# Kernel tuning notes

Hardware: AMD Instinct MI355X
Metric: run time of the kernel (lower is better)

## Reference

```python
import jax, jax.numpy as jnp
import numpy as np

B, S, D, H = 2, 2048, 1024, 16
DK = D // H

def setup_inputs() -> dict:
    key = jax.random.key(0)
    ks = jax.random.split(key, 8)
    scale = 1.0 / np.sqrt(D)
    return {
        "q": jax.random.normal(ks[0], (B, S, D), jnp.float32),
        "k": jax.random.normal(ks[1], (B, S, D), jnp.float32),
        "v": jax.random.normal(ks[2], (B, S, D), jnp.float32),
        "reaches": jax.random.uniform(ks[3], (B, S), jnp.float32),
        "Wq": jax.random.normal(ks[4], (D, D), jnp.float32) * scale,
        "Wk": jax.random.normal(ks[5], (D, D), jnp.float32) * scale,
        "Wv": jax.random.normal(ks[6], (D, D), jnp.float32) * scale,
        "Wo": jax.random.normal(ks[7], (D, D), jnp.float32) * scale,
    }

def _split_heads(x):
    # [B,S,D] -> [B,H,S,DK]
    return x.reshape(B, S, H, DK).transpose(0, 2, 1, 3)

def reference(q, k, v, reaches, Wq, Wk, Wv, Wo):
    # torch Linear: y = x @ W.T
    qh = _split_heads(q @ Wq.T)
    kh = _split_heads(k @ Wk.T)
    vh = _split_heads(v @ Wv.T)
    scores = jnp.einsum("bhqd,bhkd->bhqk", qh, kh) / jnp.sqrt(jnp.float32(DK))
    scores = jax.nn.softmax(scores, axis=-1)
    # post-softmax reach weighting along key axis
    scores = scores * reaches[:, None, None, :]
    # diagonal suppression: scores - scores*0.999999*eye
    scores = scores * (1.0 - 0.999999 * jnp.eye(S, dtype=scores.dtype))
    # inverted combine
    out = vh - jnp.einsum("bhqk,bhkd->bhqd", scores, vh)
    # per-position contribution rescale
    rs = reaches.sum(axis=-1, keepdims=True)
    contrib = (rs - reaches) / (rs + 1e-9) * (1.0 - reaches) * 100.0  # [B,S]
    out = out * contrib[:, None, :, None]
    concat = out.transpose(0, 2, 1, 3).reshape(B, S, D)
    return concat @ Wo.T
```

## Files before the change

### kernel.cpp

```cpp
#include <hip/hip_runtime.h>
#include <hip/hip_bf16.h>

typedef __attribute__((ext_vector_type(8))) short short8;
typedef __attribute__((ext_vector_type(4))) float f32x4;
typedef __attribute__((ext_vector_type(16))) float f32x16;
typedef unsigned short us;

#define B_ 2
#define S_ 2048
#define D_ 1024
#define H_ 16
#define DK_ 64
#define QSCALE 0.1803368867f

__device__ __forceinline__ us f2bf(float f) {
  union { float f; unsigned u; } x; x.f = f;
  unsigned r = x.u + 0x7FFFu + ((x.u >> 16) & 1u);
  return (us)(r >> 16);
}
__device__ __forceinline__ float bf2f(us h) {
  union { unsigned u; float f; } x; x.u = ((unsigned)h) << 16;
  return x.f;
}
__device__ __forceinline__ us f2bf_hw(float f) {
  __hip_bfloat16 h = __float2bfloat16(f);
  return *reinterpret_cast<us*>(&h);
}
__device__ __forceinline__ unsigned cvtpk(float lo, float hi) {
  unsigned r;
  asm("v_cvt_pk_bf16_f32 %0, %1, %2" : "=v"(r) : "v"(lo), "v"(hi));
  return r;
}

__device__ __forceinline__ void gload16(const void* g, void* l) {
  __builtin_amdgcn_global_load_lds((const __attribute__((address_space(1))) void*)g,
                                   (__attribute__((address_space(3))) void*)l, 16, 0, 0);
}

__global__ __launch_bounds__(256) void cvt_all(const float* __restrict__ q,
                                               const float* __restrict__ k,
                                               const float* __restrict__ v,
                                               const float* __restrict__ Wq,
                                               const float* __restrict__ Wk,
                                               const float* __restrict__ Wv,
                                               const float* __restrict__ Wo,
                                               us* __restrict__ oq, us* __restrict__ ok,
                                               us* __restrict__ ov, us* __restrict__ oWq,
                                               us* __restrict__ oWk, us* __restrict__ oWv,
                                               us* __restrict__ oWo) {
  int bid = blockIdx.x;
  const float* in; us* out; int off;
  if (bid < 12288) {
    int t = bid >> 12;
    in = (t == 0) ? q : (t == 1) ? k : v;
    out = (t == 0) ? oq : (t == 1) ? ok : ov;
    off = (bid & 4095) * 1024;
  } else {
    int t = (bid - 12288) >> 10;
    in = (t == 0) ? Wq : (t == 1) ? Wk : (t == 2) ? Wv : Wo;
    out = (t == 0) ? oWq : (t == 1) ? oWk : (t == 2) ? oWv : oWo;
    off = ((bid - 12288) & 1023) * 1024;
  }
  int i = off + threadIdx.x * 4;
  float4 val = *reinterpret_cast<const float4*>(in + i);
  ushort4 o;
  o.x = f2bf(val.x); o.y = f2bf(val.y); o.z = f2bf(val.z); o.w = f2bf(val.w);
  *reinterpret_cast<ushort4*>(out + i) = o;
}

__global__ __launch_bounds__(256) void rs_kernel(const float* __restrict__ reaches,
                                                 float* __restrict__ rs) {
  int b = blockIdx.x, t = threadIdx.x;
  float s = 0.f;
  for (int i = t; i < S_; i += 256) s += reaches[b * S_ + i];
  for (int o = 32; o > 0; o >>= 1) s += __shfl_down(s, o, 64);
  __shared__ float tmp[4];
  if ((t & 63) == 0) tmp[t >> 6] = s;
  __syncthreads();
  if (t == 0) rs[b] = tmp[0] + tmp[1] + tmp[2] + tmp[3];
}

__device__ __forceinline__ void gemm_core_hs(const us* __restrict__ A, const us* __restrict__ Bt,
                                             us* __restrict__ outH, float oscale) {
  __shared__ __align__(16) us lA[128 * 32];
  __shared__ __align__(16) us lB[128 * 32];
  const int tid = threadIdx.x;
  const int bm = blockIdx.x >> 3, bn = blockIdx.x & 7;
  const int w = tid >> 6, lane = tid & 63;
  const int wr = (w >> 1) * 64, wc = (w & 1) * 64;
  const int lr = lane & 15, lg = lane >> 4;

  f32x4 acc[4][4];
#pragma unroll
  for (int i = 0; i < 4; ++i)
#pragma unroll
    for (int j = 0; j < 4; ++j) acc[i][j] = (f32x4){0.f, 0.f, 0.f, 0.f};

  const int crow = lane >> 2, ce8 = (lane & 3) * 8;
  const us* A0 = A + (size_t)(bm * 128 + w * 32 + crow) * 1024 + ce8;
  const us* A1 = A0 + (size_t)16 * 1024;
  const us* B0 = Bt + (size_t)(bn * 128 + w * 32 + crow) * 1024 + ce8;
  const us* B1 = B0 + (size_t)16 * 1024;
  us* lA0 = &lA[(w * 2) * 512]; us* lA1 = lA0 + 512;
  us* lB0 = &lB[(w * 2) * 512]; us* lB1 = lB0 + 512;

  for (int kt = 0; kt < 1024; kt += 32) {
    gload16(A0 + kt, lA0);
    gload16(A1 + kt, lA1);
    gload16(B0 + kt, lB0);
    gload16(B1 + kt, lB1);
    __syncthreads();
    short8 af[4], bfr[4];
#pragma unroll
    for (int i = 0; i < 4; ++i)
      af[i] = *reinterpret_cast<const short8*>(&lA[(wr + i * 16 + lr) * 32 + lg * 8]);
#pragma unroll
    for (int j = 0; j < 4; ++j)
      bfr[j] = *reinterpret_cast<const short8*>(&lB[(wc + j * 16 + lr) * 32 + lg * 8]);
#pragma unroll
    for (int i = 0; i < 4; ++i)
#pragma unroll
      for (int j = 0; j < 4; ++j)
        acc[i][j] = __builtin_amdgcn_mfma_f32_16x16x32_bf16(af[i], bfr[j], acc[i][j], 0, 0, 0);
    __syncthreads();
  }
#pragma unroll
  for (int i = 0; i < 4; ++i)
#pragma unroll
    for (int j = 0; j < 4; ++j)
#pragma unroll
      for (int ii = 0; ii < 4; ++ii) {
        int r = bm * 128 + wr + i * 16 + lg * 4 + ii;
        int c = bn * 128 + wc + j * 16 + lr;
        float v = acc[i][j][ii] * oscale;
        int b = r >> 11, s = r & (S_ - 1), h = c >> 6, dk = c & 63;
        outH[(((size_t)(b * H_ + h) * S_ + s) * DK_) + dk] = f2bf(v);
      }
}

__global__ __launch_bounds__(256) void proj_gemm(const us* __restrict__ q_bf,
                                                 const us* __restrict__ k_bf,
                                                 const us* __restrict__ v_bf,
                                                 const us* __restrict__ Wq_bf,
                                                 const us* __restrict__ Wk_bf,
                                                 const us* __restrict__ Wv_bf,
                                                 us* __restrict__ Qh, us* __restrict__ Kh,
                                                 us* __restrict__ Vh) {
  if (blockIdx.y == 0) gemm_core_hs(q_bf, Wq_bf, Qh, QSCALE);
  else if (blockIdx.y == 1) gemm_core_hs(k_bf, Wk_bf, Kh, 1.0f);
  else gemm_core_hs(v_bf, Wv_bf, Vh, 1.0f);
}

__global__ __launch_bounds__(256) void wo_gemm(const us* __restrict__ A,
                                               const us* __restrict__ Bt,
                                               float* __restrict__ outF) {
  __shared__ __align__(16) us lA[128 * 32];
  __shared__ __align__(16) us lB[64 * 32];
  const int tid = threadIdx.x;
  const int bm = blockIdx.x >> 4, bn = blockIdx.x & 15;
  const int w = tid >> 6, lane = tid & 63;
  const int lr = lane & 15, lg = lane >> 4;

  f32x4 acc[2][4];
#pragma unroll
  for (int i = 0; i < 2; ++i)
#pragma unroll
    for (int j = 0; j < 4; ++j) acc[i][j] = (f32x4){0.f, 0.f, 0.f, 0.f};

  const int crow = lane >> 2, ce8 = (lane & 3) * 8;
  const us* A0 = A + (size_t)(bm * 128 + w * 32 + crow) * 1024 + ce8;
  const us* A1 = A0 + (size_t)16 * 1024;
  const us* B0 = Bt + (size_t)(bn * 64 + w * 16 + crow) * 1024 + ce8;
  us* lA0 = &lA[w * 1024]; us* lA1 = lA0 + 512;
  us* lB0 = &lB[w * 512];

  for (int kt = 0; kt < 1024; kt += 32) {
    gload16(A0 + kt, lA0);
    gload16(A1 + kt, lA1);
    gload16(B0 + kt, lB0);
    __syncthreads();
    short8 af[2], bfr[4];
#pragma unroll
    for (int i = 0; i < 2; ++i)
      af[i] = *reinterpret_cast<const short8*>(&lA[(w * 32 + i * 16 + lr) * 32 + lg * 8]);
#pragma unroll
    for (int j = 0; j < 4; ++j)
      bfr[j] = *reinterpret_cast<const short8*>(&lB[(j * 16 + lr) * 32 + lg * 8]);
#pragma unroll
    for (int i = 0; i < 2; ++i)
#pragma unroll
      for (int j = 0; j < 4; ++j)
        acc[i][j] = __builtin_amdgcn_mfma_f32_16x16x32_bf16(af[i], bfr[j], acc[i][j], 0, 0, 0);
    __syncthreads();
  }
#pragma unroll
  for (int i = 0; i < 2; ++i)
#pragma unroll
    for (int j = 0; j < 4; ++j)
#pragma unroll
      for (int ii = 0; ii < 4; ++ii) {
        int r = bm * 128 + w * 32 + i * 16 + lg * 4 + ii;
        int c = bn * 64 + j * 16 + lr;
        outF[(size_t)r * 1024 + c] = acc[i][j][ii];
      }
}

__global__ __launch_bounds__(256) void transp_kernel(const us* __restrict__ Vh,
                                                     const float* __restrict__ reaches,
                                                     us* __restrict__ VhTw) {
  __shared__ us t[64 * 68];
  const int bh = blockIdx.x >> 5, st = blockIdx.x & 31;
  const int b = bh >> 4;
  const size_t base = (size_t)bh * S_ * DK_;
  const int r = threadIdx.x >> 3, e8 = (threadIdx.x & 7) * 8;
#pragma unroll
  for (int h2 = 0; h2 < 2; ++h2) {
    int row = r + h2 * 32;
    *reinterpret_cast<short8*>(&t[row * 68 + e8]) =
        *reinterpret_cast<const short8*>(&Vh[base + (size_t)(st * 64 + row) * DK_ + e8]);
  }
  __syncthreads();
#pragma unroll
  for (int h2 = 0; h2 < 2; ++h2) {
    int dk = (threadIdx.x >> 3) + h2 * 32;
    int sc = (threadIdx.x & 7) * 8;
    short8 v;
#pragma unroll
    for (int j = 0; j < 8; ++j) {
      float rw = reaches[b * S_ + st * 64 + sc + j];
      v[j] = (short)f2bf_hw(bf2f(t[(sc + j) * 68 + dk]) * rw);
    }
    *reinterpret_cast<short8*>(&VhTw[base + (size_t)dk * S_ + st * 64 + sc]) = v;
  }
}

__global__ __launch_bounds__(256, 2) void attn_kernel(const us* __restrict__ Qh,
                                                      const us* __restrict__ Kh,
                                                      const us* __restrict__ Vh,
                                                      const us* __restrict__ VhTw,
                                                      const float* __restrict__ reaches,
                                                      const float* __restrict__ rsum,
                                                      us* __restrict__ concat) {
  __shared__ __align__(16) us lK2[2][64 * 64];
  __shared__ __align__(16) us vT2[2][64 * 64];
  __shared__ float diagP[128];
  __shared__ float lsum[128];

  const int tid = threadIdx.x;
  const int bid = ((blockIdx.x & 7) << 6) | (blockIdx.x >> 3);
  const int qt = bid & 15;
  const int bh = bid >> 4;
  const int b = bh >> 4, h = bh & 15;
  const size_t base = (size_t)bh * S_ * DK_;

  const int w = tid >> 6, lane = tid & 63;
  const int l31 = lane & 31, hh = lane >> 5, l7 = lane & 7;
  const int h4 = hh * 4;
  const int r2 = tid >> 3, e8 = (tid & 7) * 8;
  const int diagkt = qt * 2 + (w >> 1);

  short8 aq[4];
  {
    const us* qp = &Qh[base + (size_t)(qt * 128 + w * 32 + l31) * DK_ + hh * 8];
#pragma unroll
    for (int dk = 0; dk < 4; ++dk)
      aq[dk] = *reinterpret_cast<const short8*>(qp + dk * 16);
  }

  int rdK[2][4];
#pragma unroll
  for (int c = 0; c < 2; ++c)
#pragma unroll
    for (int dk = 0; dk < 4; ++dk)
      rdK[c][dk] = (c * 32 + l31) * 64 + (((dk * 2 + hh) ^ l7) << 3);
  const int wslot = ((tid & 7) ^ (r2 & 7)) << 3;
  const int wK0 = r2 * 64 + wslot, wK1 = (r2 + 32) * 64 + wslot;

  short8 pk0, pk1, pv0, pv1;
  pk0 = *reinterpret_cast<const short8*>(&Kh[base + (size_t)r2 * DK_ + e8]);
  pk1 = *reinterpret_cast<const short8*>(&Kh[base + (size_t)(r2 + 32) * DK_ + e8]);
  pv0 = *reinterpret_cast<const short8*>(&VhTw[base + (size_t)r2 * S_ + e8]);
  pv1 = *reinterpret_cast<const short8*>(&VhTw[base + (size_t)(r2 + 32) * S_ + e8]);
  *reinterpret_cast<short8*>(&lK2[0][wK0]) = pk0;
  *reinterpret_cast<short8*>(&lK2[0][wK1]) = pk1;
  *reinterpret_cast<short8*>(&vT2[0][wK0]) = pv0;
  *reinterpret_cast<short8*>(&vT2[0][wK1]) = pv1;
  __syncthreads();

  f32x16 oacc[2];
  float lacc = 0.f;
#pragma unroll
  for (int c = 0; c < 2; ++c)
#pragma unroll
    for (int r = 0; r < 16; ++r) oacc[c][r] = 0.f;

  for (int kt = 0; kt < 32; ++kt) {
    const int cur = kt & 1;
    if (kt < 31) {
      int nt = kt + 1;
      pk0 = *reinterpret_cast<const short8*>(&Kh[base + (size_t)(nt * 64 + r2) * DK_ + e8]);
      pk1 = *reinterpret_cast<const short8*>(&Kh[base + (size_t)(nt * 64 + r2 + 32) * DK_ + e8]);
      pv0 = *reinterpret_cast<const short8*>(&VhTw[base + (size_t)r2 * S_ + nt * 64 + e8]);
      pv1 = *reinterpret_cast<const short8*>(&VhTw[base + (size_t)(r2 + 32) * S_ + nt * 64 + e8]);
    }

    f32x16 st0, st1;
#pragma unroll
    for (int r = 0; r < 16; ++r) { st0[r] = 0.f; st1[r] = 0.f; }
    __builtin_amdgcn_s_setprio(1);
#pragma unroll
    for (int dk = 0; dk < 4; ++dk) {
      short8 k0 = *reinterpret_cast<const short8*>(&lK2[cur][rdK[0][dk]]);
      st0 = __builtin_amdgcn_mfma_f32_32x32x16_bf16(k0, aq[dk], st0, 0, 0, 0);
      short8 k1 = *reinterpret_cast<const short8*>(&lK2[cur][rdK[1][dk]]);
      st1 = __builtin_amdgcn_mfma_f32_32x32x16_bf16(k1, aq[dk], st1, 0, 0, 0);
    }
    __builtin_amdgcn_s_setprio(0);

    float e0[16], e1[16];
#pragma unroll
    for (int r = 0; r < 16; ++r) {
      e0[r] = __builtin_amdgcn_exp2f(st0[r]);
      e1[r] = __builtin_amdgcn_exp2f(st1[r]);
      lacc += e0[r] + e1[r];
    }
    if (kt == diagkt) {
#pragma unroll
      for (int r = 0; r < 16; ++r) {
        int kk = (r & 3) + 8 * (r >> 2) + 4 * hh;
        float ev = (w & 1) ? e1[r] : e0[r];
        if (kk == l31) diagP[w * 32 + l31] = ev;
      }
    }

    short8 pa[4];
#pragma unroll
    for (int ks = 0; ks < 4; ++ks) {
      const int ro = (ks & 1) * 8;
      unsigned d0, s0, d1, s1;
      if (ks < 2) {
        d0 = cvtpk(e0[ro + 0], e0[ro + 1]);
        s0 = cvtpk(e0[ro + 4], e0[ro + 5]);
        d1 = cvtpk(e0[ro + 2], e0[ro + 3]);
        s1 = cvtpk(e0[ro + 6], e0[ro + 7]);
      } else {
        d0 = cvtpk(e1[ro + 0], e1[ro + 1]);
        s0 = cvtpk(e1[ro + 4], e1[ro + 5]);
        d1 = cvtpk(e1[ro + 2], e1[ro + 3]);
        s1 = cvtpk(e1[ro + 6], e1[ro + 7]);
      }
      asm("v_permlane32_swap_b32 %0, %1" : "+v"(d0), "+v"(s0));
      asm("v_permlane32_swap_b32 %0, %1" : "+v"(d1), "+v"(s1));
      union { unsigned u[4]; short8 v; } pk;
      pk.u[0] = d0; pk.u[1] = d1; pk.u[2] = s0; pk.u[3] = s1;
      pa[ks] = pk.v;
    }

    __builtin_amdgcn_s_setprio(1);
#pragma unroll
    for (int dc = 0; dc < 2; ++dc)
#pragma unroll
      for (int ks = 0; ks < 4; ++ks) {
        short8 bv = *reinterpret_cast<const short8*>(&vT2[cur][rdK[dc][ks]]);
        oacc[dc] = __builtin_amdgcn_mfma_f32_32x32x16_bf16(pa[ks], bv, oacc[dc], 0, 0, 0);
      }
    __builtin_amdgcn_s_setprio(0);

    if (kt < 31) {
      const int nx = cur ^ 1;
      *reinterpret_cast<short8*>(&lK2[nx][wK0]) = pk0;
      *reinterpret_cast<short8*>(&lK2[nx][wK1]) = pk1;
      *reinterpret_cast<short8*>(&vT2[nx][wK0]) = pv0;
      *reinterpret_cast<short8*>(&vT2[nx][wK1]) = pv1;
    }
    __syncthreads();
  }

  lacc += __shfl_xor(lacc, 32, 64);
  if (hh == 0) lsum[w * 32 + l31] = lacc;
  __syncthreads();

  const float rb = rsum[b];
#pragma unroll
  for (int r = 0; r < 16; ++r) {
    const int q = w * 32 + (r & 3) + 8 * (r >> 2) + h4;
    const int qg = qt * 128 + q;
    const float rq = reaches[b * S_ + qg];
    const float contrib = (rb - rq) / (rb + 1e-9f) * (1.f - rq) * 100.f;
    const float corr = 0.999999f * diagP[q] * rq;
    const float linv = 1.0f / lsum[q];
#pragma unroll
    for (int dc = 0; dc < 2; ++dc) {
      int d = dc * 32 + l31;
      float vhv = bf2f(Vh[base + (size_t)qg * DK_ + d]);
      float pv = (oacc[dc][r] - corr * vhv) * linv;
      float o = (vhv - pv) * contrib;
      concat[((size_t)(b * S_ + qg)) * D_ + h * 64 + d] = f2bf(o);
    }
  }
}

extern "C" void kernel_launch(void* const* d_in, const int* in_sizes, int n_in,
                              void* d_out, int out_size, void* d_ws, size_t ws_size,
                              hipStream_t stream) {
  const float* q = (const float*)d_in[0];
  const float* k = (const float*)d_in[1];
  const float* v = (const float*)d_in[2];
  const float* reaches = (const float*)d_in[3];
  const float* Wq = (const float*)d_in[4];
  const float* Wk = (const float*)d_in[5];
  const float* Wv = (const float*)d_in[6];
  const float* Wo = (const float*)d_in[7];

  const size_t NQKV = (size_t)B_ * S_ * D_;
  const size_t NW = (size_t)D_ * D_;

  us* q_bf = (us*)d_ws;
  us* k_bf = q_bf + NQKV;
  us* v_bf = k_bf + NQKV;
  us* Wq_bf = v_bf + NQKV;
  us* Wk_bf = Wq_bf + NW;
  us* Wv_bf = Wk_bf + NW;
  us* Wo_bf = Wv_bf + NW;
  us* Qh = Wo_bf + NW;
  us* Kh = Qh + NQKV;
  us* Vh = Kh + NQKV;
  us* concat = Vh + NQKV;
  float* rs = (float*)(concat + NQKV);
  us* VhTw = q_bf;

  cvt_all<<<16384, 256, 0, stream>>>(q, k, v, Wq, Wk, Wv, Wo,
                                     q_bf, k_bf, v_bf, Wq_bf, Wk_bf, Wv_bf, Wo_bf);
  rs_kernel<<<B_, 256, 0, stream>>>(reaches, rs);

  proj_gemm<<<dim3(256, 3), 256, 0, stream>>>(q_bf, k_bf, v_bf, Wq_bf, Wk_bf, Wv_bf, Qh, Kh, Vh);
  transp_kernel<<<B_ * H_ * (S_ / 64), 256, 0, stream>>>(Vh, reaches, VhTw);

  attn_kernel<<<B_ * H_ * (S_ / 128), 256, 0, stream>>>(Qh, Kh, Vh, VhTw, reaches, rs, concat);

  wo_gemm<<<512, 256, 0, stream>>>(concat, Wo_bf, (float*)d_out);
}
```

Measured before the change: 133.1 us.

## Triple-buffer LDS with async direct-to-LDS loads in GEMMs and attention

Replaces the load-then-sync loops in the projection GEMM, output GEMM and attention kernel with a three-stage LDS ring. Tiles for step k+1 are issued as direct global-to-LDS loads while step k computes. A single barrier per iteration, guarded by explicit vmcnt waits, replaces the two syncthreads. In the attention kernel this also drops the register-staged prefetch and LDS stores, and uses swizzled global addresses so the direct loads land in the existing XOR layout. The cost is three times the LDS footprint, which can lower occupancy, and correctness now depends on hand-counted vmcnt values and on the ring depth preventing overwrite races.

New measurement: 133.2 us. About the same (+0.1%).

```diff
diff --git a/kernel.cpp b/kernel.cpp
--- a/kernel.cpp
+++ b/kernel.cpp
@@ -82,8 +82,8 @@
 
 __device__ __forceinline__ void gemm_core_hs(const us* __restrict__ A, const us* __restrict__ Bt,
                                              us* __restrict__ outH, float oscale) {
-  __shared__ __align__(16) us lA[128 * 32];
-  __shared__ __align__(16) us lB[128 * 32];
+  __shared__ __align__(16) us lA[3][128 * 32];
+  __shared__ __align__(16) us lB[3][128 * 32];
   const int tid = threadIdx.x;
   const int bm = blockIdx.x >> 3, bn = blockIdx.x & 7;
   const int w = tid >> 6, lane = tid & 63;
@@ -101,28 +101,45 @@
   const us* A1 = A0 + (size_t)16 * 1024;
   const us* B0 = Bt + (size_t)(bn * 128 + w * 32 + crow) * 1024 + ce8;
   const us* B1 = B0 + (size_t)16 * 1024;
-  us* lA0 = &lA[(w * 2) * 512]; us* lA1 = lA0 + 512;
-  us* lB0 = &lB[(w * 2) * 512]; us* lB1 = lB0 + 512;
-
-  for (int kt = 0; kt < 1024; kt += 32) {
-    gload16(A0 + kt, lA0);
-    gload16(A1 + kt, lA1);
-    gload16(B0 + kt, lB0);
-    gload16(B1 + kt, lB1);
-    __syncthreads();
+  const int dA0 = (w * 32) * 32, dA1 = (w * 32 + 16) * 32;
+
+  gload16(A0, &lA[0][dA0]);
+  gload16(A1, &lA[0][dA1]);
+  gload16(B0, &lB[0][dA0]);
+  gload16(B1, &lB[0][dA1]);
+
+  int cur = 0, nxt = 1;
+  for (int kt = 0; kt < 32; ++kt) {
+    if (kt < 31) {
+      int ko = (kt + 1) * 32;
+      gload16(A0 + ko, &lA[nxt][dA0]);
+      gload16(A1 + ko, &lA[nxt][dA1]);
+      gload16(B0 + ko, &lB[nxt][dA0]);
+      gload16(B1 + ko, &lB[nxt][dA1]);
+      asm volatile("s_waitcnt vmcnt(4)" ::: "memory");
+    } else {
+      asm volatile("s_waitcnt vmcnt(0)" ::: "memory");
+    }
+    __builtin_amdgcn_s_barrier();
+    __builtin_amdgcn_sched_barrier(0);
+
     short8 af[4], bfr[4];
 #pragma unroll
     for (int i = 0; i < 4; ++i)
-      af[i] = *reinterpret_cast<const short8*>(&lA[(wr + i * 16 + lr) * 32 + lg * 8]);
+      af[i] = *reinterpret_cast<const short8*>(&lA[cur][(wr + i * 16 + lr) * 32 + lg * 8]);
 #pragma unroll
     for (int j = 0; j < 4; ++j)
-      bfr[j] = *reinterpret_cast<const short8*>(&lB[(wc + j * 16 + lr) * 32 + lg * 8]);
+      bfr[j] = *reinterpret_cast<const short8*>(&lB[cur][(wc + j * 16 + lr) * 32 + lg * 8]);
+    __builtin_amdgcn_s_setprio(1);
 #pragma unroll
     for (int i = 0; i < 4; ++i)
 #pragma unroll
       for (int j = 0; j < 4; ++j)
         acc[i][j] = __builtin_amdgcn_mfma_f32_16x16x32_bf16(af[i], bfr[j], acc[i][j], 0, 0, 0);
-    __syncthreads();
+    __builtin_amdgcn_s_setprio(0);
+
+    cur = nxt;
+    nxt = (nxt == 2) ? 0 : nxt + 1;
   }
 #pragma unroll
   for (int i = 0; i < 4; ++i)
@@ -154,8 +171,8 @@
 __global__ __launch_bounds__(256) void wo_gemm(const us* __restrict__ A,
                                                const us* __restrict__ Bt,
                                                float* __restrict__ outF) {
-  __shared__ __align__(16) us lA[128 * 32];
-  __shared__ __align__(16) us lB[64 * 32];
+  __shared__ __align__(16) us lA[3][128 * 32];
+  __shared__ __align__(16) us lB[3][64 * 32];
   const int tid = threadIdx.x;
   const int bm = blockIdx.x >> 4, bn = blockIdx.x & 15;
   const int w = tid >> 6, lane = tid & 63;
@@ -171,27 +188,43 @@
   const us* A0 = A + (size_t)(bm * 128 + w * 32 + crow) * 1024 + ce8;
   const us* A1 = A0 + (size_t)16 * 1024;
   const us* B0 = Bt + (size_t)(bn * 64 + w * 16 + crow) * 1024 + ce8;
-  us* lA0 = &lA[w * 1024]; us* lA1 = lA0 + 512;
-  us* lB0 = &lB[w * 512];
-
-  for (int kt = 0; kt < 1024; kt += 32) {
-    gload16(A0 + kt, lA0);
-    gload16(A1 + kt, lA1);
-    gload16(B0 + kt, lB0);
-    __syncthreads();
+  const int dA0 = (w * 32) * 32, dA1 = (w * 32 + 16) * 32, dB0 = (w * 16) * 32;
+
+  gload16(A0, &lA[0][dA0]);
+  gload16(A1, &lA[0][dA1]);
+  gload16(B0, &lB[0][dB0]);
+
+  int cur = 0, nxt = 1;
+  for (int kt = 0; kt < 32; ++kt) {
+    if (kt < 31) {
+      int ko = (kt + 1) * 32;
+      gload16(A0 + ko, &lA[nxt][dA0]);
+      gload16(A1 + ko, &lA[nxt][dA1]);
+      gload16(B0 + ko, &lB[nxt][dB0]);
+      asm volatile("s_waitcnt vmcnt(3)" ::: "memory");
+    } else {
+      asm volatile("s_waitcnt vmcnt(0)" ::: "memory");
+    }
+    __builtin_amdgcn_s_barrier();
+    __builtin_amdgcn_sched_barrier(0);
+
     short8 af[2], bfr[4];
 #pragma unroll
     for (int i = 0; i < 2; ++i)
-      af[i] = *reinterpret_cast<const short8*>(&lA[(w * 32 + i * 16 + lr) * 32 + lg * 8]);
+      af[i] = *reinterpret_cast<const short8*>(&lA[cur][(w * 32 + i * 16 + lr) * 32 + lg * 8]);
 #pragma unroll
     for (int j = 0; j < 4; ++j)
-      bfr[j] = *reinterpret_cast<const short8*>(&lB[(j * 16 + lr) * 32 + lg * 8]);
+      bfr[j] = *reinterpret_cast<const short8*>(&lB[cur][(j * 16 + lr) * 32 + lg * 8]);
+    __builtin_amdgcn_s_setprio(1);
 #pragma unroll
     for (int i = 0; i < 2; ++i)
 #pragma unroll
       for (int j = 0; j < 4; ++j)
         acc[i][j] = __builtin_amdgcn_mfma_f32_16x16x32_bf16(af[i], bfr[j], acc[i][j], 0, 0, 0);
-    __syncthreads();
+    __builtin_amdgcn_s_setprio(0);
+
+    cur = nxt;
+    nxt = (nxt == 2) ? 0 : nxt + 1;
   }
 #pragma unroll
   for (int i = 0; i < 2; ++i)
@@ -241,8 +274,7 @@
                                                       const float* __restrict__ reaches,
                                                       const float* __restrict__ rsum,
                                                       us* __restrict__ concat) {
-  __shared__ __align__(16) us lK2[2][64 * 64];
-  __shared__ __align__(16) us vT2[2][64 * 64];
+  __shared__ __align__(16) us sbuf[3][8192];
   __shared__ float diagP[128];
   __shared__ float lsum[128];
 
@@ -256,8 +288,16 @@
   const int w = tid >> 6, lane = tid & 63;
   const int l31 = lane & 31, hh = lane >> 5, l7 = lane & 7;
   const int h4 = hh * 4;
-  const int r2 = tid >> 3, e8 = (tid & 7) * 8;
   const int diagkt = qt * 2 + (w >> 1);
+
+  const int Lrow = lane >> 3;
+  const int cswz = (l7 ^ Lrow) << 3;
+  const us* Kg0 = Kh + base + (size_t)(w * 16 + Lrow) * DK_ + cswz;
+  const us* Kg1 = Kg0 + (size_t)8 * DK_;
+  const us* Vg0 = VhTw + base + (size_t)(w * 16 + Lrow) * S_ + cswz;
+  const us* Vg1 = Vg0 + (size_t)8 * S_;
+  const int dK0 = (w * 16) * 64, dK1 = (w * 16 + 8) * 64;
+  const int dV0 = 4096 + dK0, dV1 = 4096 + dK1;
 
   short8 aq[4];
   {
@@ -273,19 +313,11 @@
 #pragma unroll
     for (int dk = 0; dk < 4; ++dk)
       rdK[c][dk] = (c * 32 + l31) * 64 + (((dk * 2 + hh) ^ l7) << 3);
-  const int wslot = ((tid & 7) ^ (r2 & 7)) << 3;
-  const int wK0 = r2 * 64 + wslot, wK1 = (r2 + 32) * 64 + wslot;
-
-  short8 pk0, pk1, pv0, pv1;
-  pk0 = *reinterpret_cast<const short8*>(&Kh[base + (size_t)r2 * DK_ + e8]);
-  pk1 = *reinterpret_cast<const short8*>(&Kh[base + (size_t)(r2 + 32) * DK_ + e8]);
-  pv0 = *reinterpret_cast<const short8*>(&VhTw[base + (size_t)r2 * S_ + e8]);
-  pv1 = *reinterpret_cast<const short8*>(&VhTw[base + (size_t)(r2 + 32) * S_ + e8]);
-  *reinterpret_cast<short8*>(&lK2[0][wK0]) = pk0;
-  *reinterpret_cast<short8*>(&lK2[0][wK1]) = pk1;
-  *reinterpret_cast<short8*>(&vT2[0][wK0]) = pv0;
-  *reinterpret_cast<short8*>(&vT2[0][wK1]) = pv1;
-  __syncthreads();
+
+  gload16(Kg0, &sbuf[0][dK0]);
+  gload16(Kg1, &sbuf[0][dK1]);
+  gload16(Vg0, &sbuf[0][dV0]);
+  gload16(Vg1, &sbuf[0][dV1]);
 
   f32x16 oacc[2];
   float lacc = 0.f;
@@ -294,15 +326,23 @@
 #pragma unroll
     for (int r = 0; r < 16; ++r) oacc[c][r] = 0.f;
 
+  int cur = 0, nxt = 1;
   for (int kt = 0; kt < 32; ++kt) {
-    const int cur = kt & 1;
     if (kt < 31) {
-      int nt = kt + 1;
-      pk0 = *reinterpret_cast<const short8*>(&Kh[base + (size_t)(nt * 64 + r2) * DK_ + e8]);
-      pk1 = *reinterpret_cast<const short8*>(&Kh[base + (size_t)(nt * 64 + r2 + 32) * DK_ + e8]);
-      pv0 = *reinterpret_cast<const short8*>(&VhTw[base + (size_t)r2 * S_ + nt * 64 + e8]);
-      pv1 = *reinterpret_cast<const short8*>(&VhTw[base + (size_t)(r2 + 32) * S_ + nt * 64 + e8]);
-    }
+      const size_t ko = (size_t)(kt + 1) * 64;
+      gload16(Kg0 + ko * DK_, &sbuf[nxt][dK0]);
+      gload16(Kg1 + ko * DK_, &sbuf[nxt][dK1]);
+      gload16(Vg0 + ko, &sbuf[nxt][dV0]);
+      gload16(Vg1 + ko, &sbuf[nxt][dV1]);
+      asm volatile("s_waitcnt vmcnt(4)" ::: "memory");
+    } else {
+      asm volatile("s_waitcnt vmcnt(0)" ::: "memory");
+    }
+    __builtin_amdgcn_s_barrier();
+    __builtin_amdgcn_sched_barrier(0);
+
+    const us* lKc = &sbuf[cur][0];
+    const us* vTc = &sbuf[cur][4096];
 
     f32x16 st0, st1;
 #pragma unroll
@@ -310,9 +350,9 @@
     __builtin_amdgcn_s_setprio(1);
 #pragma unroll
     for (int dk = 0; dk < 4; ++dk) {
-      short8 k0 = *reinterpret_cast<const short8*>(&lK2[cur][rdK[0][dk]]);
+      short8 k0 = *reinterpret_cast<const short8*>(&lKc[rdK[0][dk]]);
       st0 = __builtin_amdgcn_mfma_f32_32x32x16_bf16(k0, aq[dk], st0, 0, 0, 0);
-      short8 k1 = *reinterpret_cast<const short8*>(&lK2[cur][rdK[1][dk]]);
+      short8 k1 = *reinterpret_cast<const short8*>(&lKc[rdK[1][dk]]);
       st1 = __builtin_amdgcn_mfma_f32_32x32x16_bf16(k1, aq[dk], st1, 0, 0, 0);
     }
     __builtin_amdgcn_s_setprio(0);
@@ -361,19 +401,13 @@
     for (int dc = 0; dc < 2; ++dc)
 #pragma unroll
       for (int ks = 0; ks < 4; ++ks) {
-        short8 bv = *reinterpret_cast<const short8*>(&vT2[cur][rdK[dc][ks]]);
+        short8 bv = *reinterpret_cast<const short8*>(&vTc[rdK[dc][ks]]);
         oacc[dc] = __builtin_amdgcn_mfma_f32_32x32x16_bf16(pa[ks], bv, oacc[dc], 0, 0, 0);
       }
     __builtin_amdgcn_s_setprio(0);
 
-    if (kt < 31) {
-      const int nx = cur ^ 1;
-      *reinterpret_cast<short8*>(&lK2[nx][wK0]) = pk0;
-      *reinterpret_cast<short8*>(&lK2[nx][wK1]) = pk1;
-      *reinterpret_cast<short8*>(&vT2[nx][wK0]) = pv0;
-      *reinterpret_cast<short8*>(&vT2[nx][wK1]) = pv1;
-    }
-    __syncthreads();
+    cur = nxt;
+    nxt = (nxt == 2) ? 0 : nxt + 1;
   }
 
   lacc += __shfl_xor(lacc, 32, 64);
```
